# Kernel optimization log

Measured on AMD Instinct MI355X. Metric: run time of the kernel, lower is better.

## Reference

```python
import jax, jax.numpy as jnp
import numpy as np

V, E, H, L = 10000, 300, 256, 9   # vocab, embed_dim, hidden_dim, num_labels
B, T = 128, 512                   # batch, seq_len


def setup_inputs() -> dict:
    key = jax.random.key(0)
    ks = jax.random.split(key, 14)
    s = 0.05
    emb = jax.random.normal(ks[2], (V, E), jnp.float32) * s
    emb = emb.at[0].set(0.0)  # padding_idx=0
    return {
        "input_ids": jax.random.randint(ks[0], (B, T), 0, V),
        "attention_mask": jnp.ones((B, T), jnp.int32),
        "labels": jax.random.randint(ks[1], (B, T), 0, L),
        "emb": emb,
        "Wih_f": jax.random.normal(ks[3], (4 * H, E), jnp.float32) * s,
        "Whh_f": jax.random.normal(ks[4], (4 * H, H), jnp.float32) * s,
        "b_f": jnp.zeros((4 * H,), jnp.float32),
        "Wih_b": jax.random.normal(ks[5], (4 * H, E), jnp.float32) * s,
        "Whh_b": jax.random.normal(ks[6], (4 * H, H), jnp.float32) * s,
        "b_b": jnp.zeros((4 * H,), jnp.float32),
        "Wc": jax.random.normal(ks[7], (L, 2 * H), jnp.float32) * s,
        "bc": jnp.zeros((L,), jnp.float32),
        "transitions": jax.random.normal(ks[8], (L, L), jnp.float32) * 0.1,
        "start_trans": jax.random.normal(ks[9], (L,), jnp.float32) * 0.1,
        "end_trans": jax.random.normal(ks[10], (L,), jnp.float32) * 0.1,
    }


def _lstm_dir(x, Wih, Whh, b):
    # x: (T, B, E) -> hidden states (T, B, H); PyTorch gate order i,f,g,o
    Bn = x.shape[1]
    h0 = jnp.zeros((Bn, Whh.shape[1]), x.dtype)
    c0 = jnp.zeros((Bn, Whh.shape[1]), x.dtype)
    # precompute input projections once (big GEMM), scan only does small HxH GEMM
    xp = jnp.einsum('tbe,ge->tbg', x, Wih) + b
    def step(carry, xg):
        h, c = carry
        g = xg + h @ Whh.T
        i, f, gg, o = jnp.split(g, 4, axis=-1)
        c = jax.nn.sigmoid(f) * c + jax.nn.sigmoid(i) * jnp.tanh(gg)
        h = jax.nn.sigmoid(o) * jnp.tanh(c)
        return (h, c), h
    _, hs = jax.lax.scan(step, (h0, c0), xp)
    return hs


def reference(input_ids, attention_mask, labels, emb, Wih_f, Whh_f, b_f,
              Wih_b, Whh_b, b_b, Wc, bc, transitions, start_trans, end_trans):
    x = emb[input_ids]                       # (B, T, E)
    xt = jnp.transpose(x, (1, 0, 2))         # (T, B, E)
    hf = _lstm_dir(xt, Wih_f, Whh_f, b_f)
    hb = _lstm_dir(xt[::-1], Wih_b, Whh_b, b_b)[::-1]
    h = jnp.concatenate([hf, hb], axis=-1)   # (T, B, 2H); dropout is identity in eval
    em = h @ Wc.T + bc                       # (T, B, L) emissions

    mask = jnp.transpose(attention_mask, (1, 0)).astype(bool)  # (T, B)
    tags = jnp.transpose(labels, (1, 0))                        # (T, B)
    Bn = em.shape[1]
    bidx = jnp.arange(Bn)

    # --- numerator: score of gold path (torchcrf._compute_score) ---
    score0 = start_trans[tags[0]] + em[0, bidx, tags[0]]
    def num_step(carry, inp):
        score, prev = carry
        e_t, t_t, m_t = inp
        score = score + (transitions[prev, t_t] + e_t[bidx, t_t]) * m_t
        return (score, t_t), None
    (score, _), _ = jax.lax.scan(
        num_step, (score0, tags[0]),
        (em[1:], tags[1:], mask[1:].astype(em.dtype)))
    seq_ends = mask.astype(jnp.int32).sum(0) - 1
    last_tags = tags[seq_ends, bidx]
    score = score + end_trans[last_tags]

    # --- denominator: log partition (torchcrf._compute_normalizer) ---
    alpha0 = start_trans + em[0]             # (B, L)
    def den_step(alpha, inp):
        e_t, m_t = inp
        nxt = jax.nn.logsumexp(alpha[:, :, None] + transitions[None] + e_t[:, None, :], axis=1)
        return jnp.where(m_t[:, None], nxt, alpha), None
    alpha, _ = jax.lax.scan(den_step, alpha0, (em[1:], mask[1:]))
    logZ = jax.nn.logsumexp(alpha + end_trans, axis=-1)

    llh = score - logZ
    return -jnp.mean(llh)  # crf(..., reduction='mean'), negated
```

## Files before the change

kernel.cpp:

```cpp
#include <hip/hip_runtime.h>
#include <hip/hip_bf16.h>

#define Vn 10000
#define En 300
#define Hn 256
#define Gn 1024
#define Ln 9
#define Bn 128
#define Tn 512

#if defined(__has_builtin)
#  if __has_builtin(__builtin_amdgcn_sdot8)
#    define HAS_SDOT8 1
#  endif
#endif
#ifndef HAS_SDOT8
#  define HAS_SDOT8 0
#endif

static __device__ __forceinline__ float bf2f(unsigned short u) {
    return __uint_as_float(((unsigned int)u) << 16);
}
static __device__ __forceinline__ unsigned short f2bf(float f) {
    unsigned int x = __float_as_uint(f);
    return (unsigned short)((x + 0x7FFFu + ((x >> 16) & 1u)) >> 16);
}
static __device__ __forceinline__ float sigm(float x) {
    return 1.f / (1.f + __expf(-x));
}
static __device__ __forceinline__ float tanh_fast(float x) {
    return 2.f / (1.f + __expf(-2.f * x)) - 1.f;
}
static __device__ __forceinline__ int dot8(unsigned int w, int h, int acc) {
#if HAS_SDOT8
    return __builtin_amdgcn_sdot8((int)w, h, acc, false);
#else
    unsigned int wl = ((w & 0x0F0F0F0Fu) ^ 0x08080808u) - 0x08080808u;
    unsigned int wh = (((w >> 4) & 0x0F0F0F0Fu) ^ 0x08080808u) - 0x08080808u;
    unsigned int hl = (((unsigned)h & 0x0F0F0F0Fu) ^ 0x08080808u) - 0x08080808u;
    unsigned int hh = ((((unsigned)h >> 4) & 0x0F0F0F0Fu) ^ 0x08080808u) - 0x08080808u;
    acc = __builtin_amdgcn_sdot4((int)wl, (int)hl, acc, false);
    return __builtin_amdgcn_sdot4((int)wh, (int)hh, acc, false);
#endif
}

__global__ __launch_bounds__(256) void k_transpose_wih(
    const float* __restrict__ Wf, const float* __restrict__ Wb,
    float* __restrict__ Tf, float* __restrict__ Tb) {
    int n = blockIdx.x * 256 + threadIdx.x;
    const float* src = blockIdx.y ? Wb : Wf;
    float* dst = blockIdx.y ? Tb : Tf;
    int e = n / Gn, j = n % Gn;
    dst[n] = src[j * En + e];
}

__global__ __launch_bounds__(64) void k_quant_whh(
    const float* __restrict__ Wf, const float* __restrict__ Wb,
    unsigned int* __restrict__ qr_f, unsigned int* __restrict__ ql_f,
    unsigned int* __restrict__ qr_b, unsigned int* __restrict__ ql_b,
    float* __restrict__ scl_f, float* __restrict__ scl_b) {
    int j = blockIdx.x;
    int dir = blockIdx.y;
    int lane = threadIdx.x;
    const float* W = dir ? Wb : Wf;
    float w8[8];
    float m = 0.f;
    if (lane < 32) {
        float4 wlo = *(const float4*)&W[(size_t)j * Hn + 8 * lane];
        float4 whi = *(const float4*)&W[(size_t)j * Hn + 8 * lane + 4];
        w8[0] = wlo.x; w8[1] = wlo.y; w8[2] = wlo.z; w8[3] = wlo.w;
        w8[4] = whi.x; w8[5] = whi.y; w8[6] = whi.z; w8[7] = whi.w;
        #pragma unroll
        for (int i = 0; i < 8; ++i) m = fmaxf(m, fabsf(w8[i]));
    }
    #pragma unroll
    for (int sft = 32; sft >= 1; sft >>= 1) m = fmaxf(m, __shfl_xor(m, sft, 64));
    float inv = (m > 0.f) ? (7.f / m) : 0.f;
    if (lane < 32) {
        unsigned int d = 0;
        #pragma unroll
        for (int i = 0; i < 8; ++i) {
            int qi = (int)rintf(w8[i] * inv);
            d |= ((unsigned int)(qi & 0xF)) << (4 * i);
        }
        if (lane < 16)
            (dir ? qr_b : qr_f)[(size_t)((lane >> 2) * 1024 + j) * 4 + (lane & 3)] = d;
        else {
            int e = lane - 16;
            (dir ? ql_b : ql_f)[(size_t)((e >> 2) * 1024 + j) * 4 + (e & 3)] = d;
        }
    }
    if (lane == 0) (dir ? scl_b : scl_f)[j] = m / 49.f;
}

__global__ __launch_bounds__(256) void k_proj(
    const float* __restrict__ emb,
    const float* __restrict__ WihT_f, const float* __restrict__ WihT_b,
    const float* __restrict__ b_f, const float* __restrict__ b_b,
    unsigned short* __restrict__ Pf, unsigned short* __restrict__ Pb) {
    int tid = threadIdx.x;
    int tx = tid & 63, ty = tid >> 6;
    int dir = blockIdx.z;
    const float* WT = dir ? WihT_b : WihT_f;
    const float* bias = dir ? b_b : b_f;
    unsigned short* P = dir ? Pb : Pf;
    int v0 = blockIdx.x * 32 + ty * 8;
    int j0 = blockIdx.y * 256 + tx * 4;
    const float* erow[8];
    #pragma unroll
    for (int r = 0; r < 8; ++r) {
        int vr = v0 + r; if (vr > Vn - 1) vr = Vn - 1;
        erow[r] = emb + (size_t)vr * En;
    }
    float4 acc[8];
    #pragma unroll
    for (int r = 0; r < 8; ++r) acc[r] = make_float4(0.f, 0.f, 0.f, 0.f);
    for (int e0 = 0; e0 < En; e0 += 4) {
        float4 w0 = *(const float4*)&WT[(size_t)(e0 + 0) * Gn + j0];
        float4 w1 = *(const float4*)&WT[(size_t)(e0 + 1) * Gn + j0];
        float4 w2 = *(const float4*)&WT[(size_t)(e0 + 2) * Gn + j0];
        float4 w3 = *(const float4*)&WT[(size_t)(e0 + 3) * Gn + j0];
        #pragma unroll
        for (int r = 0; r < 8; ++r) {
            float4 a = *(const float4*)&erow[r][e0];
            acc[r].x += a.x*w0.x + a.y*w1.x + a.z*w2.x + a.w*w3.x;
            acc[r].y += a.x*w0.y + a.y*w1.y + a.z*w2.y + a.w*w3.y;
            acc[r].z += a.x*w0.z + a.y*w1.z + a.z*w2.z + a.w*w3.z;
            acc[r].w += a.x*w0.w + a.y*w1.w + a.z*w2.w + a.w*w3.w;
        }
    }
    float4 bb = *(const float4*)&bias[j0];
    #pragma unroll
    for (int r = 0; r < 8; ++r) {
        if (v0 + r < Vn) {
            ushort4 o;
            o.x = f2bf(acc[r].x + bb.x); o.y = f2bf(acc[r].y + bb.y);
            o.z = f2bf(acc[r].z + bb.z); o.w = f2bf(acc[r].w + bb.w);
            *(ushort4*)&P[(size_t)(v0 + r) * Gn + j0] = o;
        }
    }
}

__global__ __launch_bounds__(1024, 4) void k_lstm(
    const int* __restrict__ ids,
    const uint4* __restrict__ qr_f, const uint4* __restrict__ ql_f,
    const uint4* __restrict__ qr_b, const uint4* __restrict__ ql_b,
    const float* __restrict__ scl_f, const float* __restrict__ scl_b,
    const unsigned short* __restrict__ Pf, const unsigned short* __restrict__ Pb,
    const float* __restrict__ Wc,
    float* __restrict__ em_pf, float* __restrict__ em_pb) {
    __shared__ uint4 wlds[4 * 1024];
    __shared__ float g_stage[Gn];
    __shared__ float hstage[Hn];
    __shared__ uint4 h4v[8];
    __shared__ int ids_lds[Tn];
    __shared__ float wc_lds[Ln][Hn];
    int tid = threadIdx.x;
    int dir = blockIdx.x >> 7;
    int batch = blockIdx.x & 127;
    const uint4* qr = dir ? qr_b : qr_f;
    const uint4* ql = dir ? ql_b : ql_f;
    const unsigned short* P = dir ? Pb : Pf;
    float* em_p = dir ? em_pb : em_pf;

    unsigned int wReg[16];
    #pragma unroll
    for (int d4 = 0; d4 < 4; ++d4) {
        uint4 v = qr[(size_t)d4 * 1024 + tid];
        wReg[4*d4+0] = v.x; wReg[4*d4+1] = v.y; wReg[4*d4+2] = v.z; wReg[4*d4+3] = v.w;
        wlds[d4 * 1024 + tid] = ql[(size_t)d4 * 1024 + tid];
    }
    float sc = (dir ? scl_b : scl_f)[tid];
    if (tid < Tn) ids_lds[tid] = ids[batch * Tn + tid];
    for (int i = tid; i < Ln * Hn; i += 1024)
        wc_lds[i >> 8][i & 255] = Wc[(size_t)(i >> 8) * 512 + dir * 256 + (i & 255)];
    if (tid < 8) { uint4 z = {0u, 0u, 0u, 0u}; h4v[tid] = z; }
    float c = 0.f;
    __syncthreads();

    int t0 = dir ? (Tn - 1) : 0;
    float p = bf2f(P[(size_t)ids_lds[t0] * Gn + tid]);

    for (int s = 0; s < Tn; ++s) {
        #pragma unroll
        for (int d = 0; d < 16; ++d) asm volatile("" : "+v"(wReg[d]));

        int t = dir ? (Tn - 1 - s) : s;
        int s2 = (s + 1 < Tn) ? s + 1 : Tn - 1;
        int t2 = dir ? (Tn - 1 - s2) : s2;
        unsigned short nx = P[(size_t)ids_lds[t2] * Gn + tid];

        uint4 hq  = h4v[tid & 7];
        uint4 wv0 = wlds[tid];
        uint4 wv1 = wlds[1024 + tid];
        uint4 wv2 = wlds[2048 + tid];
        uint4 wv3 = wlds[3072 + tid];

        int acc0 = 0, acc1 = 0;
        #pragma unroll
        for (int g = 0; g < 4; ++g) {
            int h0 = __builtin_amdgcn_readlane((int)hq.x, g);
            int h1 = __builtin_amdgcn_readlane((int)hq.y, g);
            int h2 = __builtin_amdgcn_readlane((int)hq.z, g);
            int h3 = __builtin_amdgcn_readlane((int)hq.w, g);
            acc0 = dot8(wReg[4*g+0], h0, acc0);
            acc1 = dot8(wReg[4*g+1], h1, acc1);
            acc0 = dot8(wReg[4*g+2], h2, acc0);
            acc1 = dot8(wReg[4*g+3], h3, acc1);
        }
        {
            uint4 wv[4] = {wv0, wv1, wv2, wv3};
            #pragma unroll
            for (int g = 4; g < 8; ++g) {
                int h0 = __builtin_amdgcn_readlane((int)hq.x, g);
                int h1 = __builtin_amdgcn_readlane((int)hq.y, g);
                int h2 = __builtin_amdgcn_readlane((int)hq.z, g);
                int h3 = __builtin_amdgcn_readlane((int)hq.w, g);
                acc0 = dot8(wv[g-4].x, h0, acc0);
                acc1 = dot8(wv[g-4].y, h1, acc1);
                acc0 = dot8(wv[g-4].z, h2, acc0);
                acc1 = dot8(wv[g-4].w, h3, acc1);
            }
        }
        g_stage[tid] = sc * (float)(acc0 + acc1) + p;
        __syncthreads();
        if (tid < Hn) {
            float gi = g_stage[tid];
            float gf = g_stage[tid + 256];
            float gg = g_stage[tid + 512];
            float go = g_stage[tid + 768];
            float cn = sigm(gf) * c + sigm(gi) * tanh_fast(gg);
            float hn = sigm(go) * tanh_fast(cn);
            c = cn;
            hstage[tid] = hn;
            int qh = (int)rintf(7.f * hn);
            int qo = __shfl_xor(qh, 1, 64);
            if ((tid & 1) == 0)
                ((char*)h4v)[tid >> 1] = (char)((qh & 0xF) | ((qo & 0xF) << 4));
        }
        __syncthreads();
        if (tid >= 448) {
            int l = (tid >> 6) - 7;
            int lane = tid & 63;
            float4 h4 = *(const float4*)&hstage[lane * 4];
            float4 w4 = *(const float4*)&wc_lds[l][lane * 4];
            float pe = h4.x * w4.x + h4.y * w4.y + h4.z * w4.z + h4.w * w4.w;
            #pragma unroll
            for (int m = 32; m >= 1; m >>= 1) pe += __shfl_xor(pe, m, 64);
            if (lane == 0) em_p[((size_t)t * Bn + batch) * Ln + l] = pe;
        }
        p = bf2f(nx);
    }
}

__global__ __launch_bounds__(64) void k_crf_den(
    const float* __restrict__ pf, const float* __restrict__ pb,
    const float* __restrict__ bc, const int* __restrict__ mask,
    const float* __restrict__ trans, const float* __restrict__ start,
    const float* __restrict__ endt, float* __restrict__ logZ) {
    int lane = threadIdx.x;
    int grp = lane >> 5;
    int b = blockIdx.x + 64 * grp;
    int lj = lane & 31;
    int jj = (lj < Ln) ? lj : Ln - 1;
    int base = lane & 32;
    float trj[Ln];
    #pragma unroll
    for (int i = 0; i < Ln; ++i) trj[i] = trans[i * Ln + jj];
    float bcj = bc[jj];
    size_t ix0 = (size_t)b * Ln + jj;
    float alpha = start[jj] + pf[ix0] + pb[ix0] + bcj;
    size_t ix1 = (size_t)(1 * Bn + b) * Ln + jj;
    size_t ix2 = (size_t)(2 * Bn + b) * Ln + jj;
    float e1 = pf[ix1] + pb[ix1] + bcj;
    float e2 = pf[ix2] + pb[ix2] + bcj;
    int m1 = mask[b * Tn + 1];
    int m2 = mask[b * Tn + 2];
    for (int t = 1; t < Tn; ++t) {
        float s0 = __shfl(alpha, base + 0, 64) + trj[0];
        float s1 = __shfl(alpha, base + 1, 64) + trj[1];
        float s2 = __shfl(alpha, base + 2, 64) + trj[2];
        float s3 = __shfl(alpha, base + 3, 64) + trj[3];
        float s4 = __shfl(alpha, base + 4, 64) + trj[4];
        float s5 = __shfl(alpha, base + 5, 64) + trj[5];
        float s6 = __shfl(alpha, base + 6, 64) + trj[6];
        float s7 = __shfl(alpha, base + 7, 64) + trj[7];
        float s8 = __shfl(alpha, base + 8, 64) + trj[8];
        float mx = fmaxf(fmaxf(fmaxf(s0, s1), fmaxf(s2, s3)),
                         fmaxf(fmaxf(s4, s5), fmaxf(fmaxf(s6, s7), s8)));
        float sum = __expf(s0 - mx) + __expf(s1 - mx) + __expf(s2 - mx)
                  + __expf(s3 - mx) + __expf(s4 - mx) + __expf(s5 - mx)
                  + __expf(s6 - mx) + __expf(s7 - mx) + __expf(s8 - mx);
        float nxt = mx + __logf(sum) + e1;
        if (m1) alpha = nxt;
        e1 = e2; m1 = m2;
        int t2 = (t + 2 < Tn) ? t + 2 : Tn - 1;
        size_t ixn = (size_t)(t2 * Bn + b) * Ln + jj;
        e2 = pf[ixn] + pb[ixn] + bcj;
        m2 = mask[b * Tn + t2];
    }
    float s = (lj < Ln) ? alpha + endt[lj] : -1e30f;
    float mx = s;
    #pragma unroll
    for (int d = 16; d >= 1; d >>= 1) mx = fmaxf(mx, __shfl_xor(mx, d, 64));
    float sm = __expf(s - mx);
    #pragma unroll
    for (int d = 16; d >= 1; d >>= 1) sm += __shfl_xor(sm, d, 64);
    if (lj == 0) logZ[b] = mx + __logf(sm);
}

__global__ __launch_bounds__(64) void k_crf_num(
    const float* __restrict__ pf, const float* __restrict__ pb,
    const float* __restrict__ bc, const int* __restrict__ labels,
    const int* __restrict__ mask, const float* __restrict__ trans,
    const float* __restrict__ start, const float* __restrict__ endt,
    float* __restrict__ score) {
    int b = blockIdx.x, lane = threadIdx.x;
    float acc = 0.f; int cnt = 0;
    for (int t = lane; t < Tn; t += 64) {
        int tag = labels[b * Tn + t];
        int mt = mask[b * Tn + t];
        cnt += mt;
        size_t ix = (size_t)(t * Bn + b) * Ln + tag;
        float e = pf[ix] + pb[ix] + bc[tag];
        if (t == 0) {
            acc += start[tag] + e;
        } else {
            int prev = labels[b * Tn + t - 1];
            if (mt) acc += trans[prev * Ln + tag] + e;
        }
    }
    #pragma unroll
    for (int m = 32; m >= 1; m >>= 1) {
        acc += __shfl_xor(acc, m, 64);
        cnt += __shfl_xor(cnt, m, 64);
    }
    if (lane == 0) {
        int send = cnt - 1;
        int last = labels[b * Tn + send];
        score[b] = acc + endt[last];
    }
}

__global__ __launch_bounds__(128) void k_final(
    const float* __restrict__ score, const float* __restrict__ logZ,
    float* __restrict__ out) {
    __shared__ float s_s[128];
    int tid = threadIdx.x;
    s_s[tid] = score[tid] - logZ[tid];
    #pragma unroll
    for (int m = 64; m >= 1; m >>= 1) {
        __syncthreads();
        if (tid < m) s_s[tid] += s_s[tid + m];
    }
    if (tid == 0) out[0] = -s_s[0] / (float)Bn;
}

extern "C" void kernel_launch(void* const* d_in, const int* in_sizes, int n_in,
                              void* d_out, int out_size, void* d_ws, size_t ws_size,
                              hipStream_t stream) {
    const int* ids = (const int*)d_in[0];
    const int* msk = (const int*)d_in[1];
    const int* lbl = (const int*)d_in[2];
    const float* emb = (const float*)d_in[3];
    const float* Wih_f = (const float*)d_in[4];
    const float* Whh_f = (const float*)d_in[5];
    const float* b_f = (const float*)d_in[6];
    const float* Wih_b = (const float*)d_in[7];
    const float* Whh_b = (const float*)d_in[8];
    const float* b_b = (const float*)d_in[9];
    const float* Wc = (const float*)d_in[10];
    const float* bc = (const float*)d_in[11];
    const float* trans = (const float*)d_in[12];
    const float* st = (const float*)d_in[13];
    const float* en = (const float*)d_in[14];

    char* ws = (char*)d_ws;
    float* WihT_f = (float*)ws;                 ws += (size_t)En * Gn * 4;
    float* WihT_b = (float*)ws;                 ws += (size_t)En * Gn * 4;
    unsigned int* qr_f = (unsigned int*)ws;     ws += 65536;
    unsigned int* ql_f = (unsigned int*)ws;     ws += 65536;
    unsigned int* qr_b = (unsigned int*)ws;     ws += 65536;
    unsigned int* ql_b = (unsigned int*)ws;     ws += 65536;
    float* scl_f = (float*)ws;                  ws += 4096;
    float* scl_b = (float*)ws;                  ws += 4096;
    unsigned short* Pf = (unsigned short*)ws;   ws += (size_t)Vn * Gn * 2;
    unsigned short* Pb = (unsigned short*)ws;   ws += (size_t)Vn * Gn * 2;
    float* em_pf = (float*)ws;                  ws += (size_t)Tn * Bn * Ln * 4;
    float* em_pb = (float*)ws;                  ws += (size_t)Tn * Bn * Ln * 4;
    float* score = (float*)ws;                  ws += 512;
    float* logZ = (float*)ws;                   ws += 512;

    k_transpose_wih<<<dim3(1200, 2), 256, 0, stream>>>(Wih_f, Wih_b, WihT_f, WihT_b);
    k_quant_whh<<<dim3(1024, 2), 64, 0, stream>>>(Whh_f, Whh_b, qr_f, ql_f, qr_b, ql_b, scl_f, scl_b);
    k_proj<<<dim3(313, 4, 2), 256, 0, stream>>>(emb, WihT_f, WihT_b, b_f, b_b, Pf, Pb);
    k_lstm<<<256, 1024, 0, stream>>>(ids,
        (const uint4*)qr_f, (const uint4*)ql_f, (const uint4*)qr_b, (const uint4*)ql_b,
        scl_f, scl_b, Pf, Pb, Wc, em_pf, em_pb);
    k_crf_den<<<64, 64, 0, stream>>>(em_pf, em_pb, bc, msk, trans, st, en, logZ);
    k_crf_num<<<128, 64, 0, stream>>>(em_pf, em_pb, bc, lbl, msk, trans, st, en, score);
    k_final<<<1, 128, 0, stream>>>(score, logZ, (float*)d_out);
}
```

Before: 1.094 ms.

## Move emission projection out of LSTM loop and use fp16 dot2 for input projection

The per-step classifier projection (three extra waves and a barrier) is removed from the recurrent LSTM loop. Hidden states are now written as bf16 to global memory, and a separate k_emit kernel computes the emissions, including the bias, in parallel afterwards. The vocabulary input-projection GEMM now packs embeddings and weights to fp16 and uses fdot2, halving its operand traffic. The dot8 accumulators are split into four chains. This trades extra global writes and reads of the hidden states (about 64MB) and some fp16 precision loss for a shorter serial critical path.

```diff
diff --git a/kernel.cpp b/kernel.cpp
--- a/kernel.cpp
+++ b/kernel.cpp
@@ -1,8 +1,10 @@
 #include <hip/hip_runtime.h>
 #include <hip/hip_bf16.h>
+#include <hip/hip_fp16.h>
 
 #define Vn 10000
 #define En 300
+#define E2n 150
 #define Hn 256
 #define Gn 1024
 #define Ln 9
@@ -13,10 +15,18 @@
 #  if __has_builtin(__builtin_amdgcn_sdot8)
 #    define HAS_SDOT8 1
 #  endif
+#  if __has_builtin(__builtin_amdgcn_fdot2)
+#    define HAS_FDOT2 1
+#  endif
 #endif
 #ifndef HAS_SDOT8
 #  define HAS_SDOT8 0
 #endif
+#ifndef HAS_FDOT2
+#  define HAS_FDOT2 0
+#endif
+
+typedef _Float16 half2_t __attribute__((ext_vector_type(2)));
 
 static __device__ __forceinline__ float bf2f(unsigned short u) {
     return __uint_as_float(((unsigned int)u) << 16);
@@ -43,15 +53,41 @@
     return __builtin_amdgcn_sdot4((int)wh, (int)hh, acc, false);
 #endif
 }
-
-__global__ __launch_bounds__(256) void k_transpose_wih(
+static __device__ __forceinline__ float fdot2f(unsigned int a, unsigned int b, float acc) {
+#if HAS_FDOT2
+    return __builtin_amdgcn_fdot2(__builtin_bit_cast(half2_t, a),
+                                  __builtin_bit_cast(half2_t, b), acc, false);
+#else
+    half2_t av = __builtin_bit_cast(half2_t, a);
+    half2_t bv = __builtin_bit_cast(half2_t, b);
+    return acc + (float)av.x * (float)bv.x + (float)av.y * (float)bv.y;
+#endif
+}
+static __device__ __forceinline__ unsigned int packf16(float a, float b) {
+    half2_t v = {(_Float16)a, (_Float16)b};
+    return __builtin_bit_cast(unsigned int, v);
+}
+
+__global__ __launch_bounds__(256) void k_prep_emb(
+    const float* __restrict__ emb, unsigned int* __restrict__ embp) {
+    int n = blockIdx.x * 256 + threadIdx.x;
+    if (n >= Vn * E2n) return;
+    int v = n / E2n, e2 = n % E2n;
+    float a = emb[(size_t)v * En + 2 * e2];
+    float b = emb[(size_t)v * En + 2 * e2 + 1];
+    embp[n] = packf16(a, b);
+}
+
+__global__ __launch_bounds__(256) void k_prep_wt(
     const float* __restrict__ Wf, const float* __restrict__ Wb,
-    float* __restrict__ Tf, float* __restrict__ Tb) {
+    unsigned int* __restrict__ Tf, unsigned int* __restrict__ Tb) {
     int n = blockIdx.x * 256 + threadIdx.x;
     const float* src = blockIdx.y ? Wb : Wf;
-    float* dst = blockIdx.y ? Tb : Tf;
-    int e = n / Gn, j = n % Gn;
-    dst[n] = src[j * En + e];
+    unsigned int* dst = blockIdx.y ? Tb : Tf;
+    int e2 = n / Gn, j = n % Gn;
+    float a = src[(size_t)j * En + 2 * e2];
+    float b = src[(size_t)j * En + 2 * e2 + 1];
+    dst[n] = packf16(a, b);
 }
 
 __global__ __launch_bounds__(64) void k_quant_whh(
@@ -94,39 +130,33 @@
 }
 
 __global__ __launch_bounds__(256) void k_proj(
-    const float* __restrict__ emb,
-    const float* __restrict__ WihT_f, const float* __restrict__ WihT_b,
+    const unsigned int* __restrict__ embp,
+    const unsigned int* __restrict__ WT16_f, const unsigned int* __restrict__ WT16_b,
     const float* __restrict__ b_f, const float* __restrict__ b_b,
     unsigned short* __restrict__ Pf, unsigned short* __restrict__ Pb) {
     int tid = threadIdx.x;
     int tx = tid & 63, ty = tid >> 6;
     int dir = blockIdx.z;
-    const float* WT = dir ? WihT_b : WihT_f;
+    const unsigned int* WT = dir ? WT16_b : WT16_f;
     const float* bias = dir ? b_b : b_f;
     unsigned short* P = dir ? Pb : Pf;
     int v0 = blockIdx.x * 32 + ty * 8;
     int j0 = blockIdx.y * 256 + tx * 4;
-    const float* erow[8];
-    #pragma unroll
-    for (int r = 0; r < 8; ++r) {
-        int vr = v0 + r; if (vr > Vn - 1) vr = Vn - 1;
-        erow[r] = emb + (size_t)vr * En;
-    }
+    int vr[8];
+    #pragma unroll
+    for (int r = 0; r < 8; ++r) { int v = v0 + r; vr[r] = (v < Vn) ? v : Vn - 1; }
     float4 acc[8];
     #pragma unroll
     for (int r = 0; r < 8; ++r) acc[r] = make_float4(0.f, 0.f, 0.f, 0.f);
-    for (int e0 = 0; e0 < En; e0 += 4) {
-        float4 w0 = *(const float4*)&WT[(size_t)(e0 + 0) * Gn + j0];
-        float4 w1 = *(const float4*)&WT[(size_t)(e0 + 1) * Gn + j0];
-        float4 w2 = *(const float4*)&WT[(size_t)(e0 + 2) * Gn + j0];
-        float4 w3 = *(const float4*)&WT[(size_t)(e0 + 3) * Gn + j0];
+    for (int e2 = 0; e2 < E2n; ++e2) {
+        uint4 w = *(const uint4*)&WT[(size_t)e2 * Gn + j0];
         #pragma unroll
         for (int r = 0; r < 8; ++r) {
-            float4 a = *(const float4*)&erow[r][e0];
-            acc[r].x += a.x*w0.x + a.y*w1.x + a.z*w2.x + a.w*w3.x;
-            acc[r].y += a.x*w0.y + a.y*w1.y + a.z*w2.y + a.w*w3.y;
-            acc[r].z += a.x*w0.z + a.y*w1.z + a.z*w2.z + a.w*w3.z;
-            acc[r].w += a.x*w0.w + a.y*w1.w + a.z*w2.w + a.w*w3.w;
+            unsigned int a = embp[(size_t)vr[r] * E2n + e2];
+            acc[r].x = fdot2f(a, w.x, acc[r].x);
+            acc[r].y = fdot2f(a, w.y, acc[r].y);
+            acc[r].z = fdot2f(a, w.z, acc[r].z);
+            acc[r].w = fdot2f(a, w.w, acc[r].w);
         }
     }
     float4 bb = *(const float4*)&bias[j0];
@@ -147,21 +177,18 @@
     const uint4* __restrict__ qr_b, const uint4* __restrict__ ql_b,
     const float* __restrict__ scl_f, const float* __restrict__ scl_b,
     const unsigned short* __restrict__ Pf, const unsigned short* __restrict__ Pb,
-    const float* __restrict__ Wc,
-    float* __restrict__ em_pf, float* __restrict__ em_pb) {
+    unsigned short* __restrict__ hs_f, unsigned short* __restrict__ hs_b) {
     __shared__ uint4 wlds[4 * 1024];
     __shared__ float g_stage[Gn];
-    __shared__ float hstage[Hn];
     __shared__ uint4 h4v[8];
     __shared__ int ids_lds[Tn];
-    __shared__ float wc_lds[Ln][Hn];
     int tid = threadIdx.x;
     int dir = blockIdx.x >> 7;
     int batch = blockIdx.x & 127;
     const uint4* qr = dir ? qr_b : qr_f;
     const uint4* ql = dir ? ql_b : ql_f;
     const unsigned short* P = dir ? Pb : Pf;
-    float* em_p = dir ? em_pb : em_pf;
+    unsigned short* hs = dir ? hs_b : hs_f;
 
     unsigned int wReg[16];
     #pragma unroll
@@ -172,8 +199,6 @@
     }
     float sc = (dir ? scl_b : scl_f)[tid];
     if (tid < Tn) ids_lds[tid] = ids[batch * Tn + tid];
-    for (int i = tid; i < Ln * Hn; i += 1024)
-        wc_lds[i >> 8][i & 255] = Wc[(size_t)(i >> 8) * 512 + dir * 256 + (i & 255)];
     if (tid < 8) { uint4 z = {0u, 0u, 0u, 0u}; h4v[tid] = z; }
     float c = 0.f;
     __syncthreads();
@@ -182,8 +207,10 @@
     float p = bf2f(P[(size_t)ids_lds[t0] * Gn + tid]);
 
     for (int s = 0; s < Tn; ++s) {
-        #pragma unroll
-        for (int d = 0; d < 16; ++d) asm volatile("" : "+v"(wReg[d]));
+        asm volatile("" : "+v"(wReg[0]), "+v"(wReg[1]), "+v"(wReg[2]), "+v"(wReg[3]),
+                          "+v"(wReg[4]), "+v"(wReg[5]), "+v"(wReg[6]), "+v"(wReg[7]),
+                          "+v"(wReg[8]), "+v"(wReg[9]), "+v"(wReg[10]), "+v"(wReg[11]),
+                          "+v"(wReg[12]), "+v"(wReg[13]), "+v"(wReg[14]), "+v"(wReg[15]));
 
         int t = dir ? (Tn - 1 - s) : s;
         int s2 = (s + 1 < Tn) ? s + 1 : Tn - 1;
@@ -196,17 +223,17 @@
         uint4 wv2 = wlds[2048 + tid];
         uint4 wv3 = wlds[3072 + tid];
 
-        int acc0 = 0, acc1 = 0;
+        int a0 = 0, a1 = 0, a2 = 0, a3 = 0;
         #pragma unroll
         for (int g = 0; g < 4; ++g) {
             int h0 = __builtin_amdgcn_readlane((int)hq.x, g);
             int h1 = __builtin_amdgcn_readlane((int)hq.y, g);
             int h2 = __builtin_amdgcn_readlane((int)hq.z, g);
             int h3 = __builtin_amdgcn_readlane((int)hq.w, g);
-            acc0 = dot8(wReg[4*g+0], h0, acc0);
-            acc1 = dot8(wReg[4*g+1], h1, acc1);
-            acc0 = dot8(wReg[4*g+2], h2, acc0);
-            acc1 = dot8(wReg[4*g+3], h3, acc1);
+            a0 = dot8(wReg[4*g+0], h0, a0);
+            a1 = dot8(wReg[4*g+1], h1, a1);
+            a2 = dot8(wReg[4*g+2], h2, a2);
+            a3 = dot8(wReg[4*g+3], h3, a3);
         }
         {
             uint4 wv[4] = {wv0, wv1, wv2, wv3};
@@ -216,13 +243,13 @@
                 int h1 = __builtin_amdgcn_readlane((int)hq.y, g);
                 int h2 = __builtin_amdgcn_readlane((int)hq.z, g);
                 int h3 = __builtin_amdgcn_readlane((int)hq.w, g);
-                acc0 = dot8(wv[g-4].x, h0, acc0);
-                acc1 = dot8(wv[g-4].y, h1, acc1);
-                acc0 = dot8(wv[g-4].z, h2, acc0);
-                acc1 = dot8(wv[g-4].w, h3, acc1);
+                a0 = dot8(wv[g-4].x, h0, a0);
+                a1 = dot8(wv[g-4].y, h1, a1);
+                a2 = dot8(wv[g-4].z, h2, a2);
+                a3 = dot8(wv[g-4].w, h3, a3);
             }
         }
-        g_stage[tid] = sc * (float)(acc0 + acc1) + p;
+        g_stage[tid] = sc * (float)((a0 + a1) + (a2 + a3)) + p;
         __syncthreads();
         if (tid < Hn) {
             float gi = g_stage[tid];
@@ -232,30 +259,50 @@
             float cn = sigm(gf) * c + sigm(gi) * tanh_fast(gg);
             float hn = sigm(go) * tanh_fast(cn);
             c = cn;
-            hstage[tid] = hn;
+            hs[(size_t)(t * Bn + batch) * Hn + tid] = f2bf(hn);
             int qh = (int)rintf(7.f * hn);
             int qo = __shfl_xor(qh, 1, 64);
             if ((tid & 1) == 0)
                 ((char*)h4v)[tid >> 1] = (char)((qh & 0xF) | ((qo & 0xF) << 4));
         }
         __syncthreads();
-        if (tid >= 448) {
-            int l = (tid >> 6) - 7;
-            int lane = tid & 63;
-            float4 h4 = *(const float4*)&hstage[lane * 4];
-            float4 w4 = *(const float4*)&wc_lds[l][lane * 4];
-            float pe = h4.x * w4.x + h4.y * w4.y + h4.z * w4.z + h4.w * w4.w;
-            #pragma unroll
-            for (int m = 32; m >= 1; m >>= 1) pe += __shfl_xor(pe, m, 64);
-            if (lane == 0) em_p[((size_t)t * Bn + batch) * Ln + l] = pe;
-        }
         p = bf2f(nx);
     }
 }
 
+__global__ __launch_bounds__(256) void k_emit(
+    const unsigned short* __restrict__ hs_f, const unsigned short* __restrict__ hs_b,
+    const float* __restrict__ Wc, const float* __restrict__ bc,
+    float* __restrict__ em) {
+    __shared__ float wc_s[Ln * 2 * Hn];
+    int tid = threadIdx.x;
+    for (int i = tid; i < Ln * 2 * Hn; i += 256) wc_s[i] = Wc[i];
+    __syncthreads();
+    int lane = tid & 63, wid = tid >> 6;
+    int tb = blockIdx.x * 4 + wid;
+    const unsigned short* hf = hs_f + (size_t)tb * Hn;
+    const unsigned short* hb = hs_b + (size_t)tb * Hn;
+    uint2 uf = *(const uint2*)&hf[lane * 4];
+    uint2 ub = *(const uint2*)&hb[lane * 4];
+    float f0 = __uint_as_float(uf.x << 16), f1 = __uint_as_float(uf.x & 0xFFFF0000u);
+    float f2v = __uint_as_float(uf.y << 16), f3 = __uint_as_float(uf.y & 0xFFFF0000u);
+    float b0 = __uint_as_float(ub.x << 16), b1 = __uint_as_float(ub.x & 0xFFFF0000u);
+    float b2 = __uint_as_float(ub.y << 16), b3 = __uint_as_float(ub.y & 0xFFFF0000u);
+    #pragma unroll
+    for (int l = 0; l < Ln; ++l) {
+        const float* w = &wc_s[l * 2 * Hn];
+        float p = f0 * w[4 * lane] + f1 * w[4 * lane + 1]
+                + f2v * w[4 * lane + 2] + f3 * w[4 * lane + 3]
+                + b0 * w[Hn + 4 * lane] + b1 * w[Hn + 4 * lane + 1]
+                + b2 * w[Hn + 4 * lane + 2] + b3 * w[Hn + 4 * lane + 3];
+        #pragma unroll
+        for (int m = 32; m >= 1; m >>= 1) p += __shfl_xor(p, m, 64);
+        if (lane == 0) em[(size_t)tb * Ln + l] = p + bc[l];
+    }
+}
+
 __global__ __launch_bounds__(64) void k_crf_den(
-    const float* __restrict__ pf, const float* __restrict__ pb,
-    const float* __restrict__ bc, const int* __restrict__ mask,
+    const float* __restrict__ em, const int* __restrict__ mask,
     const float* __restrict__ trans, const float* __restrict__ start,
     const float* __restrict__ endt, float* __restrict__ logZ) {
     int lane = threadIdx.x;
@@ -267,13 +314,9 @@
     float trj[Ln];
     #pragma unroll
     for (int i = 0; i < Ln; ++i) trj[i] = trans[i * Ln + jj];
-    float bcj = bc[jj];
-    size_t ix0 = (size_t)b * Ln + jj;
-    float alpha = start[jj] + pf[ix0] + pb[ix0] + bcj;
-    size_t ix1 = (size_t)(1 * Bn + b) * Ln + jj;
-    size_t ix2 = (size_t)(2 * Bn + b) * Ln + jj;
-    float e1 = pf[ix1] + pb[ix1] + bcj;
-    float e2 = pf[ix2] + pb[ix2] + bcj;
+    float alpha = start[jj] + em[(size_t)b * Ln + jj];
+    float e1 = em[(size_t)(1 * Bn + b) * Ln + jj];
+    float e2 = em[(size_t)(2 * Bn + b) * Ln + jj];
     int m1 = mask[b * Tn + 1];
     int m2 = mask[b * Tn + 2];
     for (int t = 1; t < Tn; ++t) {
@@ -295,8 +338,7 @@
         if (m1) alpha = nxt;
         e1 = e2; m1 = m2;
         int t2 = (t + 2 < Tn) ? t + 2 : Tn - 1;
-        size_t ixn = (size_t)(t2 * Bn + b) * Ln + jj;
-        e2 = pf[ixn] + pb[ixn] + bcj;
+        e2 = em[(size_t)(t2 * Bn + b) * Ln + jj];
         m2 = mask[b * Tn + t2];
     }
     float s = (lj < Ln) ? alpha + endt[lj] : -1e30f;
@@ -310,8 +352,7 @@
 }
 
 __global__ __launch_bounds__(64) void k_crf_num(
-    const float* __restrict__ pf, const float* __restrict__ pb,
-    const float* __restrict__ bc, const int* __restrict__ labels,
+    const float* __restrict__ em, const int* __restrict__ labels,
     const int* __restrict__ mask, const float* __restrict__ trans,
     const float* __restrict__ start, const float* __restrict__ endt,
     float* __restrict__ score) {
@@ -321,8 +362,7 @@
         int tag = labels[b * Tn + t];
         int mt = mask[b * Tn + t];
         cnt += mt;
-        size_t ix = (size_t)(t * Bn + b) * Ln + tag;
-        float e = pf[ix] + pb[ix] + bc[tag];
+        float e = em[(size_t)(t * Bn + b) * Ln + tag];
         if (t == 0) {
             acc += start[tag] + e;
         } else {
@@ -376,8 +416,8 @@
     const float* en = (const float*)d_in[14];
 
     char* ws = (char*)d_ws;
-    float* WihT_f = (float*)ws;                 ws += (size_t)En * Gn * 4;
-    float* WihT_b = (float*)ws;                 ws += (size_t)En * Gn * 4;
+    unsigned int* WT16_f = (unsigned int*)ws;   ws += (size_t)E2n * Gn * 4;
+    unsigned int* WT16_b = (unsigned int*)ws;   ws += (size_t)E2n * Gn * 4;
     unsigned int* qr_f = (unsigned int*)ws;     ws += 65536;
     unsigned int* ql_f = (unsigned int*)ws;     ws += 65536;
     unsigned int* qr_b = (unsigned int*)ws;     ws += 65536;
@@ -386,18 +426,22 @@
     float* scl_b = (float*)ws;                  ws += 4096;
     unsigned short* Pf = (unsigned short*)ws;   ws += (size_t)Vn * Gn * 2;
     unsigned short* Pb = (unsigned short*)ws;   ws += (size_t)Vn * Gn * 2;
-    float* em_pf = (float*)ws;                  ws += (size_t)Tn * Bn * Ln * 4;
-    float* em_pb = (float*)ws;                  ws += (size_t)Tn * Bn * Ln * 4;
+    unsigned short* hs_f = (unsigned short*)ws; ws += (size_t)Tn * Bn * Hn * 2;
+    unsigned short* hs_b = (unsigned short*)ws; ws += (size_t)Tn * Bn * Hn * 2;
+    float* em = (float*)ws;                     ws += (size_t)Tn * Bn * Ln * 4;
     float* score = (float*)ws;                  ws += 512;
     float* logZ = (float*)ws;                   ws += 512;
-
-    k_transpose_wih<<<dim3(1200, 2), 256, 0, stream>>>(Wih_f, Wih_b, WihT_f, WihT_b);
+    unsigned int* embp = (unsigned int*)hs_f;
+
+    k_prep_emb<<<(Vn * E2n + 255) / 256, 256, 0, stream>>>(emb, embp);
+    k_prep_wt<<<dim3((E2n * Gn) / 256, 2), 256, 0, stream>>>(Wih_f, Wih_b, WT16_f, WT16_b);
     k_quant_whh<<<dim3(1024, 2), 64, 0, stream>>>(Whh_f, Whh_b, qr_f, ql_f, qr_b, ql_b, scl_f, scl_b);
-    k_proj<<<dim3(313, 4, 2), 256, 0, stream>>>(emb, WihT_f, WihT_b, b_f, b_b, Pf, Pb);
+    k_proj<<<dim3(313, 4, 2), 256, 0, stream>>>(embp, WT16_f, WT16_b, b_f, b_b, Pf, Pb);
     k_lstm<<<256, 1024, 0, stream>>>(ids,
         (const uint4*)qr_f, (const uint4*)ql_f, (const uint4*)qr_b, (const uint4*)ql_b,
-        scl_f, scl_b, Pf, Pb, Wc, em_pf, em_pb);
-    k_crf_den<<<64, 64, 0, stream>>>(em_pf, em_pb, bc, msk, trans, st, en, logZ);
-    k_crf_num<<<128, 64, 0, stream>>>(em_pf, em_pb, bc, lbl, msk, trans, st, en, score);
+        scl_f, scl_b, Pf, Pb, hs_f, hs_b);
+    k_emit<<<16384, 256, 0, stream>>>(hs_f, hs_b, Wc, bc, em);
+    k_crf_den<<<64, 64, 0, stream>>>(em, msk, trans, st, en, logZ);
+    k_crf_num<<<128, 64, 0, stream>>>(em, lbl, msk, trans, st, en, score);
     k_final<<<1, 128, 0, stream>>>(score, logZ, (float*)d_out);
 }
```

New measurement: 929.3 us. -15.1%, faster.
